# Kernel optimization log

Measured on AMD Instinct MI355X. Metric: run time of the kernel, lower is better.

The kernel has to match this reference:

```python
import jax, jax.numpy as jnp
import numpy as np

WS = (8, 8)  # window_size
NUM_HEADS = 6


def _relative_position_index(ws):
    ch, cw = np.arange(ws[0]), np.arange(ws[1])
    coords = np.stack(np.meshgrid(ch, cw, indexing='ij'))  # [2, Wh, Ww]
    cf = coords.reshape(2, -1)  # [2, N]
    rel = cf[:, :, None] - cf[:, None, :]  # [2, N, N]
    rel = rel.transpose(1, 2, 0).astype(np.int64)
    rel[:, :, 0] += ws[0] - 1
    rel[:, :, 1] += ws[1] - 1
    rel[:, :, 0] *= 2 * ws[1] - 1
    return rel.sum(-1)  # [N, N]

_RPI = jnp.asarray(_relative_position_index(WS))  # [64, 64] int


def setup_inputs() -> dict:
    key = jax.random.key(0)
    ks = jax.random.split(key, 6)
    B_, N, C = 4096, WS[0] * WS[1], 192
    return {
        'x': jax.random.normal(ks[0], (B_, N, C), jnp.float32),
        'qkv_w': jax.random.normal(ks[1], (3 * C, C), jnp.float32) * 0.02,
        'qkv_b': jax.random.normal(ks[2], (3 * C,), jnp.float32) * 0.02,
        'proj_w': jax.random.normal(ks[3], (C, C), jnp.float32) * 0.02,
        'proj_b': jax.random.normal(ks[4], (C,), jnp.float32) * 0.02,
        'rpb_table': jax.random.normal(ks[5], ((2 * WS[0] - 1) * (2 * WS[1] - 1), NUM_HEADS), jnp.float32) * 0.02,
    }


def reference(x, qkv_w, qkv_b, proj_w, proj_b, rpb_table):
    B_, N, C = x.shape
    H = NUM_HEADS
    D = C // H
    scale = D ** (-0.5)
    # qkv: torch Linear -> x @ W^T + b
    qkv = (x @ qkv_w.T + qkv_b).reshape(B_, N, 3, H, D)
    qkv = jnp.transpose(qkv, (2, 0, 3, 1, 4))  # [3, B_, H, N, D]
    q, k, v = qkv[0] * scale, qkv[1], qkv[2]
    attn = jnp.einsum('bhnd,bhmd->bhnm', q, k)  # [B_, H, N, N]
    bias = rpb_table[_RPI]  # [N, N, H]
    attn = attn + jnp.transpose(bias, (2, 0, 1))[None]  # broadcast over B_
    attn = jax.nn.softmax(attn, axis=-1)
    out = jnp.einsum('bhnm,bhmd->bnhd', attn, v).reshape(B_, N, C)
    return out @ proj_w.T + proj_b
```

## Files before the change

### kernel.cpp

```cpp
#include <hip/hip_runtime.h>
#include <hip/hip_bf16.h>

typedef short bf16x8 __attribute__((ext_vector_type(8)));
typedef float f32x4 __attribute__((ext_vector_type(4)));
typedef unsigned int u32;
typedef unsigned int u32x2 __attribute__((ext_vector_type(2)));

#define MFMA16 __builtin_amdgcn_mfma_f32_16x16x32_bf16
#define SCALE 0.17677669529663687f

#define OS_OFF 395520
#define WS_NEED (395520 + 100663296)

__device__ __forceinline__ unsigned short f2b(float x) {
  u32 u = __float_as_uint(x);
  u = (u + 0x7FFFu + ((u >> 16) & 1u)) >> 16;
  return (unsigned short)u;
}
__device__ __forceinline__ u32 pk2(float a, float b) {
  __hip_bfloat162 h = __float22bfloat162_rn(float2{a, b});
  return *(u32*)&h;
}
__device__ __forceinline__ uint2 pk4(f32x4 v) {
  return make_uint2(pk2(v[0], v[1]), pk2(v[2], v[3]));
}

__device__ __forceinline__ bf16x8 xpose(f32x4 a0, f32x4 a1) {
  u32 s0 = pk2(a0[0], a0[1]);
  u32 s1 = pk2(a0[2], a0[3]);
  u32 s2 = pk2(a1[0], a1[1]);
  u32 s3 = pk2(a1[2], a1[3]);
  u32x2 r0 = __builtin_amdgcn_permlane16_swap(s0, s2, false, false);
  u32x2 r1 = __builtin_amdgcn_permlane16_swap(s1, s3, false, false);
  union {
    u32 w[4];
    bf16x8 v;
  } u;
  u.w[0] = r0[0];
  u.w[1] = r1[0];
  u.w[2] = r0[1];
  u.w[3] = r1[1];
  return u.v;
}

__global__ void prep_kernel(const float* __restrict__ qkv_w, const float* __restrict__ qkv_b,
                            const float* __restrict__ proj_w, const float* __restrict__ rpb,
                            unsigned short* __restrict__ wqkv, unsigned short* __restrict__ wproj,
                            float* __restrict__ biasar, float* __restrict__ bq) {
  int i0 = blockIdx.x * blockDim.x + threadIdx.x;
  int stride = gridDim.x * blockDim.x;
  for (int i = i0; i < 576 * 192; i += stride) {
    float v = qkv_w[i];
    if (i < 192 * 192) v *= SCALE;
    wqkv[i] = f2b(v);
  }
  for (int i = i0; i < 192 * 192; i += stride) wproj[i] = f2b(proj_w[i]);
  for (int i = i0; i < 576; i += stride) {
    float v = qkv_b[i];
    if (i < 192) v *= SCALE;
    bq[i] = v;
  }
  for (int i = i0; i < 6 * 16 * 64 * 4; i += stride) {
    int r = i & 3;
    int lane = (i >> 2) & 63;
    int fid = (i >> 8) & 15;
    int h = i >> 12;
    int mt = fid >> 2, nt = fid & 3;
    int m = mt * 16 + (lane >> 4) * 4 + r;
    int n = nt * 16 + (lane & 15);
    int idx = ((n >> 3) - (m >> 3) + 7) * 15 + ((n & 7) - (m & 7) + 7);
    biasar[i] = rpb[idx * 6 + h];
  }
}

__global__ void __launch_bounds__(384, 4) win_attn6(
    const float* __restrict__ x, const unsigned short* __restrict__ wqkv,
    const float* __restrict__ biasar, const float* __restrict__ bq,
    unsigned short* __restrict__ osout) {
  __shared__ __align__(16) char smem[50176];
  const int bid = blockIdx.x;
  const int b = bid >> 1;
  const int hg = bid & 1;
  const int tid = threadIdx.x;
  const int wv = tid >> 6;
  const int hl = wv >> 1;
  const int head = hg * 3 + hl;
  const int half = wv & 1;
  const int lane = tid & 63;
  const int g = lane >> 4;
  const int c = lane & 15;
  char* xs = smem;
  char* exch = smem + 25600;

  {
    const float4* src = (const float4*)(x + (size_t)b * 12288) + tid;
    char* wdst = xs + (tid / 48) * 400 + (tid % 48) * 8;
#pragma unroll
    for (int it = 0; it < 8; ++it) {
      float4 v = src[it * 384];
      *(uint2*)(wdst + it * 3200) = make_uint2(pk2(v.x, v.y), pk2(v.z, v.w));
    }
  }
  __syncthreads();

  const char* xr = xs + c * 400 + g * 16;
#define XF(tt, kt) (*(const bf16x8*)(xr + (tt) * 6400 + (kt) * 64))

  bf16x8 qb[2];
  {
    const unsigned short* wq0 = wqkv + (size_t)(head * 32 + c) * 192 + 8 * g;
    const unsigned short* wq1 = wq0 + 16 * 192;
    f32x4 bq0 = *(const f32x4*)(bq + head * 32 + 4 * g);
    f32x4 bq1 = *(const f32x4*)(bq + head * 32 + 16 + 4 * g);
    f32x4 a00 = bq0, a01 = bq0, a10 = bq1, a11 = bq1;
#pragma unroll
    for (int kt = 0; kt < 6; ++kt) {
      bf16x8 w0 = *(const bf16x8*)(wq0 + kt * 32);
      bf16x8 w1 = *(const bf16x8*)(wq1 + kt * 32);
      bf16x8 x0 = XF(half * 2 + 0, kt);
      bf16x8 x1 = XF(half * 2 + 1, kt);
      a00 = MFMA16(w0, x0, a00, 0, 0, 0);
      a10 = MFMA16(w1, x0, a10, 0, 0, 0);
      a01 = MFMA16(w0, x1, a01, 0, 0, 0);
      a11 = MFMA16(w1, x1, a11, 0, 0, 0);
    }
    qb[0] = xpose(a00, a10);
    qb[1] = xpose(a01, a11);
  }

  bf16x8 ka[4], va[2][2];
  {
    char* ew = exch + hl * 8192 + half * 4096 + lane * 16;
    if (half == 0) {
      const unsigned short* wk0 = wqkv + (size_t)(192 + head * 32 + c) * 192 + 8 * g;
      const unsigned short* wk1 = wk0 + 16 * 192;
      f32x4 bk0 = *(const f32x4*)(bq + 192 + head * 32 + 4 * g);
      f32x4 bk1 = *(const f32x4*)(bq + 192 + head * 32 + 16 + 4 * g);
      f32x4 acc[2][4];
#pragma unroll
      for (int tt = 0; tt < 4; ++tt) {
        acc[0][tt] = bk0;
        acc[1][tt] = bk1;
      }
#pragma unroll
      for (int kt = 0; kt < 6; ++kt) {
        bf16x8 w0 = *(const bf16x8*)(wk0 + kt * 32);
        bf16x8 w1 = *(const bf16x8*)(wk1 + kt * 32);
#pragma unroll
        for (int tt = 0; tt < 4; ++tt) {
          bf16x8 xf = XF(tt, kt);
          acc[0][tt] = MFMA16(w0, xf, acc[0][tt], 0, 0, 0);
          acc[1][tt] = MFMA16(w1, xf, acc[1][tt], 0, 0, 0);
        }
      }
#pragma unroll
      for (int mt = 0; mt < 4; ++mt) {
        ka[mt] = xpose(acc[0][mt], acc[1][mt]);
        *(bf16x8*)(ew + mt * 1024) = ka[mt];
      }
    } else {
      const unsigned short* wv0 = wqkv + (size_t)(384 + head * 32 + c) * 192 + 8 * g;
      const unsigned short* wv1 = wv0 + 16 * 192;
      float bv0 = bq[384 + head * 32 + c];
      float bv1 = bq[384 + head * 32 + 16 + c];
      f32x4 acc[4][2];
#pragma unroll
      for (int tt = 0; tt < 4; ++tt) {
        acc[tt][0] = f32x4{bv0, bv0, bv0, bv0};
        acc[tt][1] = f32x4{bv1, bv1, bv1, bv1};
      }
#pragma unroll
      for (int kt = 0; kt < 6; ++kt) {
        bf16x8 w0 = *(const bf16x8*)(wv0 + kt * 32);
        bf16x8 w1 = *(const bf16x8*)(wv1 + kt * 32);
#pragma unroll
        for (int tt = 0; tt < 4; ++tt) {
          bf16x8 xf = XF(tt, kt);
          acc[tt][0] = MFMA16(xf, w0, acc[tt][0], 0, 0, 0);
          acc[tt][1] = MFMA16(xf, w1, acc[tt][1], 0, 0, 0);
        }
      }
#pragma unroll
      for (int dt = 0; dt < 2; ++dt)
#pragma unroll
        for (int kh = 0; kh < 2; ++kh) {
          va[dt][kh] = xpose(acc[2 * kh][dt], acc[2 * kh + 1][dt]);
          *(bf16x8*)(ew + (dt * 2 + kh) * 1024) = va[dt][kh];
        }
    }
  }
  __syncthreads();
  {
    const char* er = exch + hl * 8192 + (half ^ 1) * 4096 + lane * 16;
    if (half == 0) {
#pragma unroll
      for (int f = 0; f < 4; ++f) va[f >> 1][f & 1] = *(const bf16x8*)(er + f * 1024);
    } else {
#pragma unroll
      for (int f = 0; f < 4; ++f) ka[f] = *(const bf16x8*)(er + f * 1024);
    }
  }

  bf16x8 pbf[2][2];
  float linv[2];
  {
    const f32x4* bias4 = (const f32x4*)biasar + (size_t)(head * 16 + half * 2) * 64 + lane;
    f32x4 s[4][2];
#pragma unroll
    for (int mt = 0; mt < 4; ++mt)
#pragma unroll
      for (int n2 = 0; n2 < 2; ++n2)
        s[mt][n2] = MFMA16(ka[mt], qb[n2], bias4[(mt * 4 + n2) * 64], 0, 0, 0);
#pragma unroll
    for (int n2 = 0; n2 < 2; ++n2) {
      float mx = fmaxf(fmaxf(fmaxf(s[0][n2][0], s[0][n2][1]), fmaxf(s[0][n2][2], s[0][n2][3])),
                       fmaxf(fmaxf(s[1][n2][0], s[1][n2][1]), fmaxf(s[1][n2][2], s[1][n2][3])));
      mx = fmaxf(mx, fmaxf(fmaxf(fmaxf(s[2][n2][0], s[2][n2][1]), fmaxf(s[2][n2][2], s[2][n2][3])),
                           fmaxf(fmaxf(s[3][n2][0], s[3][n2][1]), fmaxf(s[3][n2][2], s[3][n2][3]))));
      mx = fmaxf(mx, __shfl_xor(mx, 16));
      mx = fmaxf(mx, __shfl_xor(mx, 32));
      float sum = 0.0f;
#pragma unroll
      for (int mt = 0; mt < 4; ++mt)
#pragma unroll
        for (int r = 0; r < 4; ++r) {
          float e = __expf(s[mt][n2][r] - mx);
          s[mt][n2][r] = e;
          sum += e;
        }
      sum += __shfl_xor(sum, 16);
      sum += __shfl_xor(sum, 32);
      linv[n2] = 1.0f / sum;
    }
#pragma unroll
    for (int n2 = 0; n2 < 2; ++n2) {
      pbf[0][n2] = xpose(s[0][n2], s[1][n2]);
      pbf[1][n2] = xpose(s[2][n2], s[3][n2]);
    }
  }

  f32x4 o[2][2];
#pragma unroll
  for (int dt = 0; dt < 2; ++dt)
#pragma unroll
    for (int n2 = 0; n2 < 2; ++n2) o[dt][n2] = (f32x4)0.0f;
#pragma unroll
  for (int mh = 0; mh < 2; ++mh)
#pragma unroll
    for (int n2 = 0; n2 < 2; ++n2)
#pragma unroll
      for (int dt = 0; dt < 2; ++dt) o[dt][n2] = MFMA16(va[dt][mh], pbf[mh][n2], o[dt][n2], 0, 0, 0);

  uint2* dst = (uint2*)osout + ((size_t)((b * 6 + head) * 2 + half) * 4) * 64 + lane;
#pragma unroll
  for (int dt = 0; dt < 2; ++dt)
#pragma unroll
    for (int n2 = 0; n2 < 2; ++n2) {
#pragma unroll
      for (int r = 0; r < 4; ++r) o[dt][n2][r] *= linv[n2];
      dst[(dt * 2 + n2) * 64] = pk4(o[dt][n2]);
    }
}

__global__ void __launch_bounds__(256, 4) proj_kernel(
    const unsigned short* __restrict__ osin, const unsigned short* __restrict__ wproj,
    const float* __restrict__ proj_b, float* __restrict__ out) {
  __shared__ __align__(16) char smem[24576];
  const int b = blockIdx.x;
  const int tid = threadIdx.x;
  const int w = tid >> 6;
  const int lane = tid & 63;
  const int g = lane >> 4;
  const int c = lane & 15;

  {
    const uint2* src = (const uint2*)osin + (size_t)b * 3072;
#pragma unroll
    for (int it = 0; it < 12; ++it) {
      int i = tid + it * 256;
      int ls = i & 63;
      int f = (i >> 6) & 3;
      int unit = i >> 8;
      int head = unit >> 1, half = unit & 1;
      int dt = f >> 1, n2 = f & 1;
      int tok = half * 32 + n2 * 16 + (ls & 15);
      int d0 = head * 32 + dt * 16 + 4 * (ls >> 4);
      uint2 v = src[i];
      *(uint2*)(smem + tok * 384 + (((d0 >> 3) ^ (tok & 7)) << 4) + (d0 & 7) * 2) = v;
    }
  }
  __syncthreads();

  f32x4 acc[4][3];
#pragma unroll
  for (int mt = 0; mt < 4; ++mt)
#pragma unroll
    for (int ft = 0; ft < 3; ++ft) acc[mt][ft] = (f32x4)0.0f;
#pragma unroll
  for (int kt = 0; kt < 6; ++kt) {
    bf16x8 wf[3];
#pragma unroll
    for (int ft = 0; ft < 3; ++ft)
      wf[ft] = *(const bf16x8*)(wproj + (size_t)(w * 48 + ft * 16 + c) * 192 + kt * 32 + 8 * g);
#pragma unroll
    for (int mt = 0; mt < 4; ++mt) {
      bf16x8 of = *(const bf16x8*)(smem + (mt * 16 + c) * 384 + (((kt * 4 + g) ^ (c & 7)) << 4));
#pragma unroll
      for (int ft = 0; ft < 3; ++ft) acc[mt][ft] = MFMA16(of, wf[ft], acc[mt][ft], 0, 0, 0);
    }
  }
  float* outb = out + (size_t)b * 12288;
#pragma unroll
  for (int ft = 0; ft < 3; ++ft) {
    float pbv = proj_b[w * 48 + ft * 16 + c];
#pragma unroll
    for (int mt = 0; mt < 4; ++mt)
#pragma unroll
      for (int r = 0; r < 4; ++r)
        outb[(mt * 16 + 4 * g + r) * 192 + w * 48 + ft * 16 + c] = acc[mt][ft][r] + pbv;
  }
}

#define XFRAGOLD(tt, kt) \
  (*(const bf16x8*)(xs + ((tt) * 16 + c) * 384 + ((((kt) * 4 + g) ^ (c & 7)) << 4)))

__global__ void __launch_bounds__(384, 3) win_attn(
    const float* __restrict__ x, const unsigned short* __restrict__ wqkv,
    const unsigned short* __restrict__ wproj, const float* __restrict__ biasar,
    const float* __restrict__ bq, const float* __restrict__ proj_b, float* __restrict__ out) {
  __shared__ __align__(16) char smem[24576];
  const int b = blockIdx.x;
  const int tid = threadIdx.x;
  const int w = tid >> 6;
  const int lane = tid & 63;
  const int g = lane >> 4;
  const int c = lane & 15;
  char* xs = smem;

  {
    const float* xb = x + (size_t)b * 12288;
#pragma unroll
    for (int it = 0; it < 8; ++it) {
      int idx = tid + it * 384;
      int tok = idx / 48, c4 = idx % 48;
      float4 v = *(const float4*)(xb + tok * 192 + c4 * 4);
      *(uint2*)(xs + tok * 384 + (((c4 >> 1) ^ (tok & 7)) << 4) + (c4 & 1) * 8) =
          make_uint2(pk2(v.x, v.y), pk2(v.z, v.w));
    }
  }
  __syncthreads();

  bf16x8 qb[4];
  {
    f32x4 acc[2][4];
#pragma unroll
    for (int dt = 0; dt < 2; ++dt)
#pragma unroll
      for (int tt = 0; tt < 4; ++tt) acc[dt][tt] = (f32x4)0.0f;
#pragma unroll
    for (int kt = 0; kt < 6; ++kt) {
      bf16x8 wf[2];
#pragma unroll
      for (int dt = 0; dt < 2; ++dt)
        wf[dt] = *(const bf16x8*)(wqkv + (size_t)(w * 32 + dt * 16 + c) * 192 + kt * 32 + 8 * g);
#pragma unroll
      for (int tt = 0; tt < 4; ++tt) {
        bf16x8 xf = XFRAGOLD(tt, kt);
#pragma unroll
        for (int dt = 0; dt < 2; ++dt) acc[dt][tt] = MFMA16(wf[dt], xf, acc[dt][tt], 0, 0, 0);
      }
    }
#pragma unroll
    for (int dt = 0; dt < 2; ++dt)
#pragma unroll
      for (int r = 0; r < 4; ++r) {
        float bv = bq[w * 32 + dt * 16 + 4 * g + r];
#pragma unroll
        for (int tt = 0; tt < 4; ++tt) acc[dt][tt][r] += bv;
      }
#pragma unroll
    for (int nt = 0; nt < 4; ++nt) qb[nt] = xpose(acc[0][nt], acc[1][nt]);
  }

  bf16x8 ka[4];
  {
    f32x4 acc[2][4];
#pragma unroll
    for (int dt = 0; dt < 2; ++dt)
#pragma unroll
      for (int tt = 0; tt < 4; ++tt) acc[dt][tt] = (f32x4)0.0f;
#pragma unroll
    for (int kt = 0; kt < 6; ++kt) {
      bf16x8 wf[2];
#pragma unroll
      for (int dt = 0; dt < 2; ++dt)
        wf[dt] =
            *(const bf16x8*)(wqkv + (size_t)(192 + w * 32 + dt * 16 + c) * 192 + kt * 32 + 8 * g);
#pragma unroll
      for (int tt = 0; tt < 4; ++tt) {
        bf16x8 xf = XFRAGOLD(tt, kt);
#pragma unroll
        for (int dt = 0; dt < 2; ++dt) acc[dt][tt] = MFMA16(wf[dt], xf, acc[dt][tt], 0, 0, 0);
      }
    }
#pragma unroll
    for (int dt = 0; dt < 2; ++dt)
#pragma unroll
      for (int r = 0; r < 4; ++r) {
        float bv = bq[192 + w * 32 + dt * 16 + 4 * g + r];
#pragma unroll
        for (int tt = 0; tt < 4; ++tt) acc[dt][tt][r] += bv;
      }
#pragma unroll
    for (int mt = 0; mt < 4; ++mt) ka[mt] = xpose(acc[0][mt], acc[1][mt]);
  }

  bf16x8 pbf[2][4];
  float linv[4];
  const f32x4* bias4 = (const f32x4*)biasar;
#pragma unroll
  for (int h = 0; h < 2; ++h) {
    f32x4 s[4][2];
#pragma unroll
    for (int mt = 0; mt < 4; ++mt)
#pragma unroll
      for (int n2 = 0; n2 < 2; ++n2) {
        int nt = h * 2 + n2;
        f32x4 t = MFMA16(ka[mt], qb[nt], (f32x4)0.0f, 0, 0, 0);
        s[mt][n2] = t + bias4[(w * 16 + mt * 4 + nt) * 64 + lane];
      }
#pragma unroll
    for (int n2 = 0; n2 < 2; ++n2) {
      int nt = h * 2 + n2;
      float mx = -1e30f;
#pragma unroll
      for (int mt = 0; mt < 4; ++mt)
#pragma unroll
        for (int r = 0; r < 4; ++r) mx = fmaxf(mx, s[mt][n2][r]);
      mx = fmaxf(mx, __shfl_xor(mx, 16));
      mx = fmaxf(mx, __shfl_xor(mx, 32));
      float sum = 0.0f;
#pragma unroll
      for (int mt = 0; mt < 4; ++mt)
#pragma unroll
        for (int r = 0; r < 4; ++r) {
          float e = __expf(s[mt][n2][r] - mx);
          s[mt][n2][r] = e;
          sum += e;
        }
      sum += __shfl_xor(sum, 16);
      sum += __shfl_xor(sum, 32);
      linv[nt] = 1.0f / sum;
    }
#pragma unroll
    for (int n2 = 0; n2 < 2; ++n2) {
      pbf[0][h * 2 + n2] = xpose(s[0][n2], s[1][n2]);
      pbf[1][h * 2 + n2] = xpose(s[2][n2], s[3][n2]);
    }
  }

  bf16x8 va[2][2];
  {
    f32x4 acc[4][2];
#pragma unroll
    for (int mt = 0; mt < 4; ++mt)
#pragma unroll
      for (int dt = 0; dt < 2; ++dt) acc[mt][dt] = (f32x4)0.0f;
#pragma unroll
    for (int kt = 0; kt < 6; ++kt) {
      bf16x8 wf[2];
#pragma unroll
      for (int dt = 0; dt < 2; ++dt)
        wf[dt] =
            *(const bf16x8*)(wqkv + (size_t)(384 + w * 32 + dt * 16 + c) * 192 + kt * 32 + 8 * g);
#pragma unroll
      for (int tt = 0; tt < 4; ++tt) {
        bf16x8 xf = XFRAGOLD(tt, kt);
#pragma unroll
        for (int dt = 0; dt < 2; ++dt) acc[tt][dt] = MFMA16(xf, wf[dt], acc[tt][dt], 0, 0, 0);
      }
    }
#pragma unroll
    for (int dt = 0; dt < 2; ++dt) {
      float bv = bq[384 + w * 32 + dt * 16 + c];
#pragma unroll
      for (int mt = 0; mt < 4; ++mt)
#pragma unroll
        for (int r = 0; r < 4; ++r) acc[mt][dt][r] += bv;
    }
#pragma unroll
    for (int dt = 0; dt < 2; ++dt)
#pragma unroll
      for (int kh = 0; kh < 2; ++kh) va[dt][kh] = xpose(acc[2 * kh][dt], acc[2 * kh + 1][dt]);
  }

  f32x4 o[2][4];
#pragma unroll
  for (int dt = 0; dt < 2; ++dt)
#pragma unroll
    for (int nt = 0; nt < 4; ++nt) o[dt][nt] = (f32x4)0.0f;
#pragma unroll
  for (int mh = 0; mh < 2; ++mh)
#pragma unroll
    for (int nt = 0; nt < 4; ++nt)
#pragma unroll
      for (int dt = 0; dt < 2; ++dt) o[dt][nt] = MFMA16(va[dt][mh], pbf[mh][nt], o[dt][nt], 0, 0, 0);
#pragma unroll
  for (int dt = 0; dt < 2; ++dt)
#pragma unroll
    for (int nt = 0; nt < 4; ++nt)
#pragma unroll
      for (int r = 0; r < 4; ++r) o[dt][nt][r] *= linv[nt];

  __syncthreads();
#pragma unroll
  for (int dt = 0; dt < 2; ++dt)
#pragma unroll
    for (int nt = 0; nt < 4; ++nt)
      *(uint2*)(xs + (nt * 16 + c) * 384 + (((w * 4 + dt * 2 + (g >> 1)) ^ (c & 7)) << 4) +
                (g & 1) * 8) =
          make_uint2(pk2(o[dt][nt][0], o[dt][nt][1]), pk2(o[dt][nt][2], o[dt][nt][3]));
  __syncthreads();

  f32x4 accP[4][2];
#pragma unroll
  for (int mt = 0; mt < 4; ++mt)
#pragma unroll
    for (int ft = 0; ft < 2; ++ft) accP[mt][ft] = (f32x4)0.0f;
#pragma unroll
  for (int kt = 0; kt < 6; ++kt) {
    bf16x8 wp[2];
#pragma unroll
    for (int ft = 0; ft < 2; ++ft)
      wp[ft] = *(const bf16x8*)(wproj + (size_t)(w * 32 + ft * 16 + c) * 192 + kt * 32 + 8 * g);
#pragma unroll
    for (int mt = 0; mt < 4; ++mt) {
      bf16x8 of = *(const bf16x8*)(xs + (mt * 16 + c) * 384 + (((kt * 4 + g) ^ (c & 7)) << 4));
#pragma unroll
      for (int ft = 0; ft < 2; ++ft) accP[mt][ft] = MFMA16(of, wp[ft], accP[mt][ft], 0, 0, 0);
    }
  }
  float pb0 = proj_b[w * 32 + c];
  float pb1 = proj_b[w * 32 + 16 + c];
  float* outb = out + (size_t)b * 12288;
#pragma unroll
  for (int mt = 0; mt < 4; ++mt)
#pragma unroll
    for (int ft = 0; ft < 2; ++ft) {
      float pbv = ft ? pb1 : pb0;
#pragma unroll
      for (int r = 0; r < 4; ++r)
        outb[(mt * 16 + 4 * g + r) * 192 + w * 32 + ft * 16 + c] = accP[mt][ft][r] + pbv;
    }
}

extern "C" void kernel_launch(void* const* d_in, const int* in_sizes, int n_in,
                              void* d_out, int out_size, void* d_ws, size_t ws_size,
                              hipStream_t stream) {
  const float* x = (const float*)d_in[0];
  const float* qkv_w = (const float*)d_in[1];
  const float* qkv_b = (const float*)d_in[2];
  const float* proj_w = (const float*)d_in[3];
  const float* proj_b = (const float*)d_in[4];
  const float* rpb = (const float*)d_in[5];
  char* ws = (char*)d_ws;
  unsigned short* wqkv = (unsigned short*)ws;
  unsigned short* wproj = (unsigned short*)(ws + 221184);
  float* biasar = (float*)(ws + 294912);
  float* bqv = (float*)(ws + 393216);

  prep_kernel<<<432, 256, 0, stream>>>(qkv_w, qkv_b, proj_w, rpb, wqkv, wproj, biasar, bqv);

  if (ws_size >= (size_t)WS_NEED) {
    unsigned short* osbuf = (unsigned short*)(ws + OS_OFF);
    win_attn6<<<8192, 384, 0, stream>>>(x, wqkv, biasar, bqv, osbuf);
    proj_kernel<<<4096, 256, 0, stream>>>(osbuf, wproj, proj_b, (float*)d_out);
  } else {
    win_attn<<<4096, 384, 0, stream>>>(x, wqkv, wproj, biasar, bqv, proj_b, (float*)d_out);
  }
}
```

Measured before the change: 317.1 us.

## Split attention into 2-head blocks with aliased shared memory and exp2 softmax

The attention kernel now runs 2 heads per block with 256 threads instead of 3 heads with 384, launching 12288 blocks. Block indices are remapped so consecutive windows stay on the same XCD. The K/V exchange buffer now reuses the x staging area, which halves shared memory and needs an extra barrier. The softmax folds log2(e) into the Q scale and the bias table so it can call exp2 directly. In exchange, each window's x tile is loaded and converted three times instead of twice.

```diff
diff --git a/kernel.cpp b/kernel.cpp
--- a/kernel.cpp
+++ b/kernel.cpp
@@ -8,6 +8,7 @@
 
 #define MFMA16 __builtin_amdgcn_mfma_f32_16x16x32_bf16
 #define SCALE 0.17677669529663687f
+#define LOG2E 1.4426950408889634f
 
 #define OS_OFF 395520
 #define WS_NEED (395520 + 100663296)
@@ -51,13 +52,13 @@
   int stride = gridDim.x * blockDim.x;
   for (int i = i0; i < 576 * 192; i += stride) {
     float v = qkv_w[i];
-    if (i < 192 * 192) v *= SCALE;
+    if (i < 192 * 192) v *= SCALE * LOG2E;
     wqkv[i] = f2b(v);
   }
   for (int i = i0; i < 192 * 192; i += stride) wproj[i] = f2b(proj_w[i]);
   for (int i = i0; i < 576; i += stride) {
     float v = qkv_b[i];
-    if (i < 192) v *= SCALE;
+    if (i < 192) v *= SCALE * LOG2E;
     bq[i] = v;
   }
   for (int i = i0; i < 6 * 16 * 64 * 4; i += stride) {
@@ -69,56 +70,58 @@
     int m = mt * 16 + (lane >> 4) * 4 + r;
     int n = nt * 16 + (lane & 15);
     int idx = ((n >> 3) - (m >> 3) + 7) * 15 + ((n & 7) - (m & 7) + 7);
-    biasar[i] = rpb[idx * 6 + h];
-  }
-}
-
-__global__ void __launch_bounds__(384, 4) win_attn6(
+    biasar[i] = rpb[idx * 6 + h] * LOG2E;
+  }
+}
+
+__global__ void __launch_bounds__(256, 4) win_attn4(
     const float* __restrict__ x, const unsigned short* __restrict__ wqkv,
     const float* __restrict__ biasar, const float* __restrict__ bq,
     unsigned short* __restrict__ osout) {
-  __shared__ __align__(16) char smem[50176];
+  __shared__ __align__(16) char smem[25600];
   const int bid = blockIdx.x;
-  const int b = bid >> 1;
-  const int hg = bid & 1;
+  const int xcd = bid & 7;
+  const int local = bid >> 3;
+  const int wl = local / 3;
+  const int hg = local - wl * 3;
+  const int b = xcd * 512 + wl;
   const int tid = threadIdx.x;
   const int wv = tid >> 6;
   const int hl = wv >> 1;
-  const int head = hg * 3 + hl;
+  const int head = hg * 2 + hl;
   const int half = wv & 1;
   const int lane = tid & 63;
   const int g = lane >> 4;
   const int c = lane & 15;
   char* xs = smem;
-  char* exch = smem + 25600;
-
-  {
-    const float4* src = (const float4*)(x + (size_t)b * 12288) + tid;
-    char* wdst = xs + (tid / 48) * 400 + (tid % 48) * 8;
-#pragma unroll
-    for (int it = 0; it < 8; ++it) {
-      float4 v = src[it * 384];
-      *(uint2*)(wdst + it * 3200) = make_uint2(pk2(v.x, v.y), pk2(v.z, v.w));
-    }
-  }
-  __syncthreads();
-
-  const char* xr = xs + c * 400 + g * 16;
-#define XF(tt, kt) (*(const bf16x8*)(xr + (tt) * 6400 + (kt) * 64))
+  char* exch = smem;
+
+  {
+    const float* xb = x + (size_t)b * 12288;
+#pragma unroll
+    for (int it = 0; it < 12; ++it) {
+      int idx = tid + it * 256;
+      int tok = idx / 48, c4 = idx - tok * 48;
+      float4 v = *(const float4*)(xb + tok * 192 + c4 * 4);
+      *(uint2*)(xs + tok * 400 + c4 * 8) = make_uint2(pk2(v.x, v.y), pk2(v.z, v.w));
+    }
+  }
+  __syncthreads();
 
   bf16x8 qb[2];
   {
     const unsigned short* wq0 = wqkv + (size_t)(head * 32 + c) * 192 + 8 * g;
     const unsigned short* wq1 = wq0 + 16 * 192;
-    f32x4 bq0 = *(const f32x4*)(bq + head * 32 + 4 * g);
-    f32x4 bq1 = *(const f32x4*)(bq + head * 32 + 16 + 4 * g);
-    f32x4 a00 = bq0, a01 = bq0, a10 = bq1, a11 = bq1;
+    f32x4 a00 = *(const f32x4*)(bq + head * 32 + 4 * g);
+    f32x4 a10 = *(const f32x4*)(bq + head * 32 + 16 + 4 * g);
+    f32x4 a01 = a00, a11 = a10;
+    const char* xr = xs + c * 400 + g * 16 + half * 12800;
 #pragma unroll
     for (int kt = 0; kt < 6; ++kt) {
+      bf16x8 x0 = *(const bf16x8*)(xr + kt * 64);
+      bf16x8 x1 = *(const bf16x8*)(xr + 6400 + kt * 64);
       bf16x8 w0 = *(const bf16x8*)(wq0 + kt * 32);
       bf16x8 w1 = *(const bf16x8*)(wq1 + kt * 32);
-      bf16x8 x0 = XF(half * 2 + 0, kt);
-      bf16x8 x1 = XF(half * 2 + 1, kt);
       a00 = MFMA16(w0, x0, a00, 0, 0, 0);
       a10 = MFMA16(w1, x0, a10, 0, 0, 0);
       a01 = MFMA16(w0, x1, a01, 0, 0, 0);
@@ -128,66 +131,79 @@
     qb[1] = xpose(a01, a11);
   }
 
-  bf16x8 ka[4], va[2][2];
-  {
-    char* ew = exch + hl * 8192 + half * 4096 + lane * 16;
+  bf16x8 ka[4], va[2][2], own[4];
+  {
+    const char* xr = xs + c * 400 + g * 16;
     if (half == 0) {
       const unsigned short* wk0 = wqkv + (size_t)(192 + head * 32 + c) * 192 + 8 * g;
       const unsigned short* wk1 = wk0 + 16 * 192;
       f32x4 bk0 = *(const f32x4*)(bq + 192 + head * 32 + 4 * g);
       f32x4 bk1 = *(const f32x4*)(bq + 192 + head * 32 + 16 + 4 * g);
-      f32x4 acc[2][4];
+      f32x4 ak[2][4];
 #pragma unroll
       for (int tt = 0; tt < 4; ++tt) {
-        acc[0][tt] = bk0;
-        acc[1][tt] = bk1;
+        ak[0][tt] = bk0;
+        ak[1][tt] = bk1;
       }
 #pragma unroll
       for (int kt = 0; kt < 6; ++kt) {
+        bf16x8 xf0 = *(const bf16x8*)(xr + kt * 64);
+        bf16x8 xf1 = *(const bf16x8*)(xr + 6400 + kt * 64);
+        bf16x8 xf2 = *(const bf16x8*)(xr + 12800 + kt * 64);
+        bf16x8 xf3 = *(const bf16x8*)(xr + 19200 + kt * 64);
         bf16x8 w0 = *(const bf16x8*)(wk0 + kt * 32);
         bf16x8 w1 = *(const bf16x8*)(wk1 + kt * 32);
-#pragma unroll
-        for (int tt = 0; tt < 4; ++tt) {
-          bf16x8 xf = XF(tt, kt);
-          acc[0][tt] = MFMA16(w0, xf, acc[0][tt], 0, 0, 0);
-          acc[1][tt] = MFMA16(w1, xf, acc[1][tt], 0, 0, 0);
-        }
-      }
-#pragma unroll
-      for (int mt = 0; mt < 4; ++mt) {
-        ka[mt] = xpose(acc[0][mt], acc[1][mt]);
-        *(bf16x8*)(ew + mt * 1024) = ka[mt];
-      }
+        ak[0][0] = MFMA16(w0, xf0, ak[0][0], 0, 0, 0);
+        ak[1][0] = MFMA16(w1, xf0, ak[1][0], 0, 0, 0);
+        ak[0][1] = MFMA16(w0, xf1, ak[0][1], 0, 0, 0);
+        ak[1][1] = MFMA16(w1, xf1, ak[1][1], 0, 0, 0);
+        ak[0][2] = MFMA16(w0, xf2, ak[0][2], 0, 0, 0);
+        ak[1][2] = MFMA16(w1, xf2, ak[1][2], 0, 0, 0);
+        ak[0][3] = MFMA16(w0, xf3, ak[0][3], 0, 0, 0);
+        ak[1][3] = MFMA16(w1, xf3, ak[1][3], 0, 0, 0);
+      }
+#pragma unroll
+      for (int mt = 0; mt < 4; ++mt) own[mt] = ka[mt] = xpose(ak[0][mt], ak[1][mt]);
     } else {
       const unsigned short* wv0 = wqkv + (size_t)(384 + head * 32 + c) * 192 + 8 * g;
       const unsigned short* wv1 = wv0 + 16 * 192;
       float bv0 = bq[384 + head * 32 + c];
       float bv1 = bq[384 + head * 32 + 16 + c];
-      f32x4 acc[4][2];
+      f32x4 av[4][2];
 #pragma unroll
       for (int tt = 0; tt < 4; ++tt) {
-        acc[tt][0] = f32x4{bv0, bv0, bv0, bv0};
-        acc[tt][1] = f32x4{bv1, bv1, bv1, bv1};
+        av[tt][0] = f32x4{bv0, bv0, bv0, bv0};
+        av[tt][1] = f32x4{bv1, bv1, bv1, bv1};
       }
 #pragma unroll
       for (int kt = 0; kt < 6; ++kt) {
+        bf16x8 xf0 = *(const bf16x8*)(xr + kt * 64);
+        bf16x8 xf1 = *(const bf16x8*)(xr + 6400 + kt * 64);
+        bf16x8 xf2 = *(const bf16x8*)(xr + 12800 + kt * 64);
+        bf16x8 xf3 = *(const bf16x8*)(xr + 19200 + kt * 64);
         bf16x8 w0 = *(const bf16x8*)(wv0 + kt * 32);
         bf16x8 w1 = *(const bf16x8*)(wv1 + kt * 32);
-#pragma unroll
-        for (int tt = 0; tt < 4; ++tt) {
-          bf16x8 xf = XF(tt, kt);
-          acc[tt][0] = MFMA16(xf, w0, acc[tt][0], 0, 0, 0);
-          acc[tt][1] = MFMA16(xf, w1, acc[tt][1], 0, 0, 0);
-        }
+        av[0][0] = MFMA16(xf0, w0, av[0][0], 0, 0, 0);
+        av[0][1] = MFMA16(xf0, w1, av[0][1], 0, 0, 0);
+        av[1][0] = MFMA16(xf1, w0, av[1][0], 0, 0, 0);
+        av[1][1] = MFMA16(xf1, w1, av[1][1], 0, 0, 0);
+        av[2][0] = MFMA16(xf2, w0, av[2][0], 0, 0, 0);
+        av[2][1] = MFMA16(xf2, w1, av[2][1], 0, 0, 0);
+        av[3][0] = MFMA16(xf3, w0, av[3][0], 0, 0, 0);
+        av[3][1] = MFMA16(xf3, w1, av[3][1], 0, 0, 0);
       }
 #pragma unroll
       for (int dt = 0; dt < 2; ++dt)
 #pragma unroll
-        for (int kh = 0; kh < 2; ++kh) {
-          va[dt][kh] = xpose(acc[2 * kh][dt], acc[2 * kh + 1][dt]);
-          *(bf16x8*)(ew + (dt * 2 + kh) * 1024) = va[dt][kh];
-        }
-    }
+        for (int kh = 0; kh < 2; ++kh)
+          own[dt * 2 + kh] = va[dt][kh] = xpose(av[2 * kh][dt], av[2 * kh + 1][dt]);
+    }
+  }
+  __syncthreads();
+  {
+    char* ew = exch + hl * 8192 + half * 4096 + lane * 16;
+#pragma unroll
+    for (int f = 0; f < 4; ++f) *(bf16x8*)(ew + f * 1024) = own[f];
   }
   __syncthreads();
   {
@@ -224,7 +240,7 @@
       for (int mt = 0; mt < 4; ++mt)
 #pragma unroll
         for (int r = 0; r < 4; ++r) {
-          float e = __expf(s[mt][n2][r] - mx);
+          float e = __builtin_exp2f(s[mt][n2][r] - mx);
           s[mt][n2][r] = e;
           sum += e;
         }
@@ -444,7 +460,7 @@
       for (int mt = 0; mt < 4; ++mt)
 #pragma unroll
         for (int r = 0; r < 4; ++r) {
-          float e = __expf(s[mt][n2][r] - mx);
+          float e = __builtin_exp2f(s[mt][n2][r] - mx);
           s[mt][n2][r] = e;
           sum += e;
         }
@@ -573,7 +589,7 @@
 
   if (ws_size >= (size_t)WS_NEED) {
     unsigned short* osbuf = (unsigned short*)(ws + OS_OFF);
-    win_attn6<<<8192, 384, 0, stream>>>(x, wqkv, biasar, bqv, osbuf);
+    win_attn4<<<12288, 256, 0, stream>>>(x, wqkv, biasar, bqv, osbuf);
     proj_kernel<<<4096, 256, 0, stream>>>(osbuf, wproj, proj_b, (float*)d_out);
   } else {
     win_attn<<<4096, 384, 0, stream>>>(x, wqkv, wproj, biasar, bqv, proj_b, (float*)d_out);
```

Result: faster. 289.3 us (-8.8%).
